# Optimization experiments

Hardware: AMD Instinct MI355X
Metric: run time of the kernel (lower is better)

Reference implementation:

```python
import jax, jax.numpy as jnp
import numpy as np

N = 50000
E = 400000
H1, H2, D = 4, 2, 64
NEG_SLOPE = 0.2
EPS = 1e-5


def _segment_softmax(alpha, dst, num_nodes):
    # alpha: [E, H], softmax over edges sharing the same dst node
    m = jax.ops.segment_max(alpha, dst, num_segments=num_nodes)  # [N, H]
    ex = jnp.exp(alpha - m[dst])
    den = jax.ops.segment_sum(ex, dst, num_segments=num_nodes)   # [N, H]
    return ex / den[dst]


def _gat_conv(x, src, dst, eattr, W, We, a_src, a_dst, a_edge, b, heads, num_nodes):
    # x: [N, Fin] -> h: [N, H, D]; eattr: [E, Fe] -> e: [E, H, D]
    h = (x @ W).reshape(num_nodes, heads, D)
    e = (eattr @ We).reshape(-1, heads, D)
    al_src = jnp.einsum('nhd,hd->nh', h, a_src)   # [N, H]
    al_dst = jnp.einsum('nhd,hd->nh', h, a_dst)   # [N, H]
    al_e = jnp.einsum('ehd,hd->eh', e, a_edge)    # [E, H]
    alpha = al_src[src] + al_dst[dst] + al_e
    alpha = jax.nn.leaky_relu(alpha, NEG_SLOPE)
    alpha = _segment_softmax(alpha, dst, num_nodes)
    msg = h[src] * alpha[:, :, None]              # [E, H, D]
    out = jax.ops.segment_sum(msg, dst, num_segments=num_nodes)
    return out.reshape(num_nodes, heads * D) + b


def _graph_norm(x, w, b, mean_scale):
    # PyG GraphNorm over the whole (single) graph
    mean = jnp.mean(x, axis=0, keepdims=True)
    out = x - mean * mean_scale
    var = jnp.mean(out * out, axis=0, keepdims=True)
    return w * out / jnp.sqrt(var + EPS) + b


def _forward(x, edge_index, edge_attr,
             W1, We1, as1, ad1, ae1, b1, gn1_w, gn1_b, gn1_ms,
             W2, We2, as2, ad2, ae2, b2, gn2_w, gn2_b, gn2_ms,
             Wc, bc):
    # add self loops (PyG default), self-loop edge_attr = mean of edge_attr
    loops = jnp.arange(N)
    src = jnp.concatenate([edge_index[0], loops])
    dst = jnp.concatenate([edge_index[1], loops])
    ea_mean = jnp.mean(edge_attr, axis=0, keepdims=True)
    eattr = jnp.concatenate([edge_attr, jnp.broadcast_to(ea_mean, (N, edge_attr.shape[1]))])

    h = _gat_conv(x, src, dst, eattr, W1, We1, as1, ad1, ae1, b1, H1, N)
    h = jax.nn.elu(_graph_norm(h, gn1_w, gn1_b, gn1_ms))
    h = _gat_conv(h, src, dst, eattr, W2, We2, as2, ad2, ae2, b2, H2, N)
    h = jax.nn.elu(_graph_norm(h, gn2_w, gn2_b, gn2_ms))
    return h @ Wc + bc


def setup_inputs() -> dict:
    key = jax.random.key(0)
    ks = jax.random.split(key, 20)
    g = lambda k, shape, fan: jax.random.normal(k, shape, jnp.float32) * (1.0 / np.sqrt(fan))
    inp = {
        'x': jax.random.normal(ks[0], (N, 3), jnp.float32),
        'edge_index': jax.random.randint(ks[1], (2, E), 0, N),
        'edge_attr': jax.random.uniform(ks[2], (E, 2), jnp.float32),
        'W1': g(ks[3], (3, H1 * D), 3),
        'We1': g(ks[4], (2, H1 * D), 2),
        'as1': g(ks[5], (H1, D), D),
        'ad1': g(ks[6], (H1, D), D),
        'ae1': g(ks[7], (H1, D), D),
        'b1': jnp.zeros((H1 * D,), jnp.float32),
        'gn1_w': jnp.ones((H1 * D,), jnp.float32),
        'gn1_b': jnp.zeros((H1 * D,), jnp.float32),
        'gn1_ms': jnp.ones((H1 * D,), jnp.float32),
        'W2': g(ks[8], (H1 * D, H2 * D), H1 * D),
        'We2': g(ks[9], (2, H2 * D), 2),
        'as2': g(ks[10], (H2, D), D),
        'ad2': g(ks[11], (H2, D), D),
        'ae2': g(ks[12], (H2, D), D),
        'b2': jnp.zeros((H2 * D,), jnp.float32),
        'gn2_w': jnp.ones((H2 * D,), jnp.float32),
        'gn2_b': jnp.zeros((H2 * D,), jnp.float32),
        'gn2_ms': jnp.ones((H2 * D,), jnp.float32),
        # classifier 128 -> 13
        'Wc': g(ks[13], (H2 * D, 13), H2 * D),
        'bc': jnp.zeros((13,), jnp.float32),
    }
    return inp


def reference(x, edge_index, edge_attr,
              W1, We1, as1, ad1, ae1, b1, gn1_w, gn1_b, gn1_ms,
              W2, We2, as2, ad2, ae2, b2, gn2_w, gn2_b, gn2_ms,
              Wc, bc):
    return _forward(x, edge_index, edge_attr,
                    W1, We1, as1, ad1, ae1, b1, gn1_w, gn1_b, gn1_ms,
                    W2, We2, as2, ad2, ae2, b2, gn2_w, gn2_b, gn2_ms,
                    Wc, bc)
```

## Files before the change

kernel.cpp:

```cpp
#include <hip/hip_runtime.h>
#include <math.h>

#define NEG_SLOPE 0.2f
#define GEPS 1e-5f

typedef __attribute__((ext_vector_type(8))) short short8;
typedef __attribute__((ext_vector_type(4))) float floatx4;

__device__ __forceinline__ float wave_reduce_sum(float v) {
#pragma unroll
    for (int o = 32; o > 0; o >>= 1) v += __shfl_down(v, o);
    return v;
}

__device__ __forceinline__ ushort f2bf(float f) {
    union { float f; unsigned int i; } c;
    c.f = f;
    unsigned int b = c.i;
    b += 0x7fffu + ((b >> 16) & 1u);
    return (ushort)(b >> 16);
}

__device__ __forceinline__ float bf2f(ushort u) {
    union { unsigned int i; float f; } c;
    c.i = (unsigned int)u << 16;
    return c.f;
}

__device__ __forceinline__ float2 unpack_bf2(unsigned int u) {
    union { unsigned int i; float f; } a, b;
    a.i = u << 16;
    b.i = u & 0xffff0000u;
    return make_float2(a.f, b.f);
}

__device__ __forceinline__ unsigned int pack_bf2(float lo, float hi) {
    return (unsigned int)f2bf(lo) | ((unsigned int)f2bf(hi) << 16);
}

__device__ __forceinline__ float lrelu(float v) {
    return (v > 0.f) ? v : v * NEG_SLOPE;
}

__device__ __forceinline__ float elu_fast(float v) {
    return (v > 0.f) ? v : (__expf(v) - 1.f);
}

__global__ __launch_bounds__(256) void k_pre(
    const float* __restrict__ W1, const float* __restrict__ as1, const float* __restrict__ ad1,
    const float* __restrict__ ea, const int* __restrict__ dst,
    const float* __restrict__ W2, const float* __restrict__ We1,
    const float* __restrict__ ae1, const float* __restrict__ We2,
    const float* __restrict__ ae2,
    float* __restrict__ ea_sum, int* __restrict__ deg, uint4* __restrict__ Bfrag,
    float* __restrict__ C1, float* __restrict__ C2, float* __restrict__ Ps,
    float* __restrict__ Pd, int E) {
    int b = blockIdx.x;
    if (b < 16) {
        int t = b * 256 + threadIdx.x;
        int c = t >> 9, kk = (t >> 6) & 7, L = t & 63;
        int q = L >> 4, n = c * 16 + (L & 15);
        int k0 = kk * 32 + q * 8;
        unsigned int u0 = pack_bf2(W2[(k0 + 0) * 128 + n], W2[(k0 + 1) * 128 + n]);
        unsigned int u1 = pack_bf2(W2[(k0 + 2) * 128 + n], W2[(k0 + 3) * 128 + n]);
        unsigned int u2 = pack_bf2(W2[(k0 + 4) * 128 + n], W2[(k0 + 5) * 128 + n]);
        unsigned int u3 = pack_bf2(W2[(k0 + 6) * 128 + n], W2[(k0 + 7) * 128 + n]);
        Bfrag[t] = make_uint4(u0, u1, u2, u3);
        return;
    }
    if (b == 16) {
        int t = threadIdx.x, h = t >> 6, lane = t & 63;
        float p0 = We1[t] * ae1[t];
        float p1 = We1[256 + t] * ae1[t];
        p0 = wave_reduce_sum(p0);
        p1 = wave_reduce_sum(p1);
        if (lane == 0) { C1[h] = p0; C1[4 + h] = p1; }
        float av = as1[t], dv = ad1[t];
#pragma unroll
        for (int k = 0; k < 3; ++k) {
            float wv = W1[k * 256 + t];
            float ps = wave_reduce_sum(wv * av);
            float pd = wave_reduce_sum(wv * dv);
            if (lane == 0) { Ps[h * 3 + k] = ps; Pd[h * 3 + k] = pd; }
        }
        if (t < 128) {
            float q0 = We2[t] * ae2[t];
            float q1 = We2[128 + t] * ae2[t];
            q0 = wave_reduce_sum(q0);
            q1 = wave_reduce_sum(q1);
            if (lane == 0) { C2[h] = q0; C2[2 + h] = q1; }
        }
        return;
    }
    b -= 17;
    const float2* ea2 = (const float2*)ea;
    float s0 = 0.f, s1 = 0.f;
    for (int e = b * 256 + threadIdx.x; e < E; e += 256 * 256) {
        float2 v = ea2[e];
        s0 += v.x; s1 += v.y;
        atomicAdd(&deg[dst[e]], 1);
    }
    s0 = wave_reduce_sum(s0);
    s1 = wave_reduce_sum(s1);
    if ((threadIdx.x & 63) == 0) {
        atomicAdd(&ea_sum[0], s0);
        atomicAdd(&ea_sum[1], s1);
    }
}

__global__ void k_scan1(const int* __restrict__ deg, int* __restrict__ row_ptr,
                        int* __restrict__ bsum, int N) {
    __shared__ int tmp[1024];
    int tid = threadIdx.x;
    int i = blockIdx.x * 1024 + tid;
    int v = (i < N) ? deg[i] : 0;
    tmp[tid] = v;
    __syncthreads();
#pragma unroll
    for (int off = 1; off < 1024; off <<= 1) {
        int t = (tid >= off) ? tmp[tid - off] : 0;
        __syncthreads();
        tmp[tid] += t;
        __syncthreads();
    }
    if (i < N) row_ptr[i + 1] = tmp[tid];
    if (tid == 1023) bsum[blockIdx.x] = tmp[1023];
}

__global__ void k_scan23(int* __restrict__ row_ptr, const int* __restrict__ bsum,
                         const float* __restrict__ ea_sum, const float* __restrict__ C1,
                         const float* __restrict__ C2, const float* __restrict__ Ps,
                         const float* __restrict__ Pd, const float* __restrict__ x,
                         float* __restrict__ al_s1, float* __restrict__ al_d1,
                         float* __restrict__ lE1, float* __restrict__ lE2, int N, int E) {
    __shared__ int off_s;
    int t = threadIdx.x;
    if (blockIdx.x == 0 && t >= 64 && t < 68) {
        int k = t - 64;
        float m0 = ea_sum[0] / (float)E, m1 = ea_sum[1] / (float)E;
        lE1[k] = m0 * C1[k] + m1 * C1[4 + k];
        if (k < 2) lE2[k] = m0 * C2[k] + m1 * C2[2 + k];
    }
    if (t < 64) {
        int v = (t < blockIdx.x) ? bsum[t] : 0;
#pragma unroll
        for (int o = 32; o > 0; o >>= 1) v += __shfl_xor(v, o);
        if (t == 0) off_s = v;
    }
    __syncthreads();
    int off = off_s;
    int i = blockIdx.x * 1024 + t;
    if (i == 0) row_ptr[0] = 0;
    if (i < N) {
        row_ptr[i + 1] += off;
        float x0 = x[3 * i], x1 = x[3 * i + 1], x2 = x[3 * i + 2];
        float4 sv, dv;
        sv.x = fmaf(x0, Ps[0], fmaf(x1, Ps[1], x2 * Ps[2]));
        sv.y = fmaf(x0, Ps[3], fmaf(x1, Ps[4], x2 * Ps[5]));
        sv.z = fmaf(x0, Ps[6], fmaf(x1, Ps[7], x2 * Ps[8]));
        sv.w = fmaf(x0, Ps[9], fmaf(x1, Ps[10], x2 * Ps[11]));
        dv.x = fmaf(x0, Pd[0], fmaf(x1, Pd[1], x2 * Pd[2]));
        dv.y = fmaf(x0, Pd[3], fmaf(x1, Pd[4], x2 * Pd[5]));
        dv.z = fmaf(x0, Pd[6], fmaf(x1, Pd[7], x2 * Pd[8]));
        dv.w = fmaf(x0, Pd[9], fmaf(x1, Pd[10], x2 * Pd[11]));
        *(float4*)(al_s1 + 4 * (size_t)i) = sv;
        *(float4*)(al_d1 + 4 * (size_t)i) = dv;
    }
}

__global__ void k_scatfill(const int* __restrict__ dst, const int* __restrict__ src,
                           const float* __restrict__ ea, const int* __restrict__ row_ptr,
                           int* __restrict__ deg, const float* __restrict__ al_s1,
                           const float* __restrict__ al_d1, const float* __restrict__ C1,
                           float2* __restrict__ ea2, uint4* __restrict__ wmp, int E) {
    int e = blockIdx.x * 256 + threadIdx.x;
    if (e >= E) return;
    int d = dst[e];
    int r = atomicSub(&deg[d], 1);
    int slot = row_ptr[d] + r - 1;
    int s = src[e];
    float2 v = ((const float2*)ea)[e];
    float4 as = *(const float4*)(al_s1 + 4 * (size_t)s);
    float4 ad = *(const float4*)(al_d1 + 4 * (size_t)d);
    float w0 = __expf(lrelu(as.x + ad.x + v.x * C1[0] + v.y * C1[4]));
    float w1 = __expf(lrelu(as.y + ad.y + v.x * C1[1] + v.y * C1[5]));
    float w2 = __expf(lrelu(as.z + ad.z + v.x * C1[2] + v.y * C1[6]));
    float w3 = __expf(lrelu(as.w + ad.w + v.x * C1[3] + v.y * C1[7]));
    ea2[slot] = v;
    wmp[slot] = make_uint4((unsigned int)s, pack_bf2(w0, w1), pack_bf2(w2, w3), 0u);
}

__global__ __launch_bounds__(256) void k_agg1(const float* __restrict__ x,
                                              const int* __restrict__ row_ptr,
                                              const uint4* __restrict__ wmp,
                                              const float* __restrict__ al_s,
                                              const float* __restrict__ al_d,
                                              const float* __restrict__ lE,
                                              const float* __restrict__ W1,
                                              const float* __restrict__ bias,
                                              ushort* __restrict__ out, int N) {
    int l = threadIdx.x & 31;
    int grp = threadIdx.x >> 5;
    int n = blockIdx.x * 8 + grp;
    if (n >= N) return;
    int c0 = l * 8;
    int hh = l >> 3;
    float4 wa0 = *(const float4*)(W1 + c0);
    float4 wa1 = *(const float4*)(W1 + c0 + 4);
    float4 wb0 = *(const float4*)(W1 + 256 + c0);
    float4 wb1 = *(const float4*)(W1 + 256 + c0 + 4);
    float4 wc0 = *(const float4*)(W1 + 512 + c0);
    float4 wc1 = *(const float4*)(W1 + 512 + c0 + 4);
    float4 bv0 = *(const float4*)(bias + c0);
    float4 bv1 = *(const float4*)(bias + c0 + 4);
    float4 asn = *(const float4*)(al_s + 4 * (size_t)n);
    float4 adn = *(const float4*)(al_d + 4 * (size_t)n);
    float ws0 = __expf(lrelu(asn.x + adn.x + lE[0]));
    float ws1 = __expf(lrelu(asn.y + adn.y + lE[1]));
    float ws2 = __expf(lrelu(asn.z + adn.z + lE[2]));
    float ws3 = __expf(lrelu(asn.w + adn.w + lE[3]));
    float z[12];
    float ds[4];
#pragma unroll
    for (int k = 0; k < 12; ++k) z[k] = 0.f;
#pragma unroll
    for (int k = 0; k < 4; ++k) ds[k] = 0.f;
    int i0 = row_ptr[n];
    int cnt = row_ptr[n + 1] - i0;
    for (int j = l; j < cnt; j += 32) {
        uint4 me = wmp[i0 + j];
        int s = (int)me.x;
        float xs0 = x[3 * s], xs1 = x[3 * s + 1], xs2 = x[3 * s + 2];
        float2 w01 = unpack_bf2(me.y);
        float2 w23 = unpack_bf2(me.z);
        z[0] = fmaf(w01.x, xs0, z[0]); z[1] = fmaf(w01.x, xs1, z[1]); z[2] = fmaf(w01.x, xs2, z[2]);
        z[3] = fmaf(w01.y, xs0, z[3]); z[4] = fmaf(w01.y, xs1, z[4]); z[5] = fmaf(w01.y, xs2, z[5]);
        z[6] = fmaf(w23.x, xs0, z[6]); z[7] = fmaf(w23.x, xs1, z[7]); z[8] = fmaf(w23.x, xs2, z[8]);
        z[9] = fmaf(w23.y, xs0, z[9]); z[10] = fmaf(w23.y, xs1, z[10]); z[11] = fmaf(w23.y, xs2, z[11]);
        ds[0] += w01.x; ds[1] += w01.y; ds[2] += w23.x; ds[3] += w23.y;
    }
    bool hi16 = (l & 16) != 0;
    float a0, a1, a2, a3, a4, a5, a6, a7, gv, rv;
    gv = hi16 ? z[0] : z[6];  rv = __shfl_xor(gv, 16); a0 = (hi16 ? z[6] : z[0]) + rv;
    gv = hi16 ? z[1] : z[7];  rv = __shfl_xor(gv, 16); a1 = (hi16 ? z[7] : z[1]) + rv;
    gv = hi16 ? z[2] : z[8];  rv = __shfl_xor(gv, 16); a2 = (hi16 ? z[8] : z[2]) + rv;
    gv = hi16 ? z[3] : z[9];  rv = __shfl_xor(gv, 16); a3 = (hi16 ? z[9] : z[3]) + rv;
    gv = hi16 ? z[4] : z[10]; rv = __shfl_xor(gv, 16); a4 = (hi16 ? z[10] : z[4]) + rv;
    gv = hi16 ? z[5] : z[11]; rv = __shfl_xor(gv, 16); a5 = (hi16 ? z[11] : z[5]) + rv;
    gv = hi16 ? ds[0] : ds[2]; rv = __shfl_xor(gv, 16); a6 = (hi16 ? ds[2] : ds[0]) + rv;
    gv = hi16 ? ds[1] : ds[3]; rv = __shfl_xor(gv, 16); a7 = (hi16 ? ds[3] : ds[1]) + rv;
    bool hi8 = (l & 8) != 0;
    float c0v, c1v, c2v, c3v;
    gv = hi8 ? a0 : a3; rv = __shfl_xor(gv, 8); c0v = (hi8 ? a3 : a0) + rv;
    gv = hi8 ? a1 : a4; rv = __shfl_xor(gv, 8); c1v = (hi8 ? a4 : a1) + rv;
    gv = hi8 ? a2 : a5; rv = __shfl_xor(gv, 8); c2v = (hi8 ? a5 : a2) + rv;
    gv = hi8 ? a6 : a7; rv = __shfl_xor(gv, 8); c3v = (hi8 ? a7 : a6) + rv;
#pragma unroll
    for (int o = 4; o > 0; o >>= 1) {
        c0v += __shfl_xor(c0v, o);
        c1v += __shfl_xor(c1v, o);
        c2v += __shfl_xor(c2v, o);
        c3v += __shfl_xor(c3v, o);
    }
    float wsh = (hh == 0) ? ws0 : (hh == 1) ? ws1 : (hh == 2) ? ws2 : ws3;
    float xn0 = x[3 * n], xn1 = x[3 * n + 1], xn2 = x[3 * n + 2];
    c0v = fmaf(wsh, xn0, c0v);
    c1v = fmaf(wsh, xn1, c1v);
    c2v = fmaf(wsh, xn2, c2v);
    c3v += wsh;
    float inv = 1.f / c3v;
    float v0 = fmaf(fmaf(c0v, wa0.x, fmaf(c1v, wb0.x, c2v * wc0.x)), inv, bv0.x);
    float v1 = fmaf(fmaf(c0v, wa0.y, fmaf(c1v, wb0.y, c2v * wc0.y)), inv, bv0.y);
    float v2 = fmaf(fmaf(c0v, wa0.z, fmaf(c1v, wb0.z, c2v * wc0.z)), inv, bv0.z);
    float v3 = fmaf(fmaf(c0v, wa0.w, fmaf(c1v, wb0.w, c2v * wc0.w)), inv, bv0.w);
    float v4 = fmaf(fmaf(c0v, wa1.x, fmaf(c1v, wb1.x, c2v * wc1.x)), inv, bv1.x);
    float v5 = fmaf(fmaf(c0v, wa1.y, fmaf(c1v, wb1.y, c2v * wc1.y)), inv, bv1.y);
    float v6 = fmaf(fmaf(c0v, wa1.z, fmaf(c1v, wb1.z, c2v * wc1.z)), inv, bv1.z);
    float v7 = fmaf(fmaf(c0v, wa1.w, fmaf(c1v, wb1.w, c2v * wc1.w)), inv, bv1.w);
    uint4 o;
    o.x = pack_bf2(v0, v1);
    o.y = pack_bf2(v2, v3);
    o.z = pack_bf2(v4, v5);
    o.w = pack_bf2(v6, v7);
    ((uint4*)out)[(size_t)n * 32 + l] = o;
}

__global__ __launch_bounds__(256) void k_agg2(const ushort* __restrict__ h2,
                                              const int* __restrict__ row_ptr,
                                              const uint4* __restrict__ wmp,
                                              const float2* __restrict__ ea2,
                                              const float* __restrict__ al_s,
                                              const float* __restrict__ al_d,
                                              const float* __restrict__ C2,
                                              const float* __restrict__ lE,
                                              const float* __restrict__ bias,
                                              ushort* __restrict__ out, int N) {
    int n = blockIdx.x * 4 + (threadIdx.x >> 6);
    if (n >= N) return;
    int lane = threadIdx.x & 63;
    int g = lane >> 4, c16 = lane & 15;
    bool hi = c16 >= 8;
    const uint4* h2u4 = (const uint4*)h2;
    float2 ad = *(const float2*)(al_d + 2 * (size_t)n);
    float2 as = *(const float2*)(al_s + 2 * (size_t)n);
    float wsA = __expf(lrelu(as.x + ad.x + lE[0]));
    float wsB = __expf(lrelu(as.y + ad.y + lE[1]));
    float c2x = hi ? C2[1] : C2[0];
    float c2y = hi ? C2[3] : C2[2];
    float adh = hi ? ad.y : ad.x;
    uint4 hs = h2u4[(size_t)n * 16 + c16];
    float wself = (g == 0) ? (hi ? wsB : wsA) : 0.f;
    float dsum = wself;
    float acc[8];
    {
        float2 t0 = unpack_bf2(hs.x), t1 = unpack_bf2(hs.y);
        float2 t2 = unpack_bf2(hs.z), t3 = unpack_bf2(hs.w);
        acc[0] = wself * t0.x; acc[1] = wself * t0.y;
        acc[2] = wself * t1.x; acc[3] = wself * t1.y;
        acc[4] = wself * t2.x; acc[5] = wself * t2.y;
        acc[6] = wself * t3.x; acc[7] = wself * t3.y;
    }
    int i0 = row_ptr[n];
    int cnt = row_ptr[n + 1] - i0;
    if (cnt > 0) {
        int last = cnt - 1;
        int nit = (cnt + 3) >> 2;
        int j0 = g;      float mkA = 1.f; if (j0 > last) { j0 = last; mkA = 0.f; }
        int j1 = 4 + g;  float mkB = 1.f; if (j1 > last) { j1 = last; mkB = 0.f; }
        int j2 = 8 + g;  float mkC = 1.f; if (j2 > last) { j2 = last; mkC = 0.f; }
        int j3 = 12 + g; float mkD = 1.f; if (j3 > last) { j3 = last; mkD = 0.f; }
        uint4 meA = wmp[i0 + j0]; float2 eaA = ea2[i0 + j0];
        uint4 meB = wmp[i0 + j1]; float2 eaB = ea2[i0 + j1];
        uint4 meC = wmp[i0 + j2]; float2 eaC = ea2[i0 + j2];
        uint4 meD = wmp[i0 + j3]; float2 eaD = ea2[i0 + j3];
        float2 alA = *(const float2*)(al_s + 2 * (size_t)meA.x);
        uint4 gvA = h2u4[(size_t)meA.x * 16 + c16];
        float2 alB = *(const float2*)(al_s + 2 * (size_t)meB.x);
        uint4 gvB = h2u4[(size_t)meB.x * 16 + c16];
        float2 alC = *(const float2*)(al_s + 2 * (size_t)meC.x);
        uint4 gvC = h2u4[(size_t)meC.x * 16 + c16];
        for (int it = 0; it < nit - 1; ++it) {
            float2 alD = *(const float2*)(al_s + 2 * (size_t)meD.x);
            uint4 gvD = h2u4[(size_t)meD.x * 16 + c16];
            int jn = 4 * (it + 4) + g;
            float mn = 1.f;
            if (jn > last) { jn = last; mn = 0.f; }
            uint4 meE = wmp[i0 + jn]; float2 eaE = ea2[i0 + jn];
            float lg = (hi ? alA.y : alA.x) + adh + eaA.x * c2x + eaA.y * c2y;
            float wg = __expf(lrelu(lg)) * mkA;
            dsum += wg;
            float2 u;
            u = unpack_bf2(gvA.x); acc[0] = fmaf(wg, u.x, acc[0]); acc[1] = fmaf(wg, u.y, acc[1]);
            u = unpack_bf2(gvA.y); acc[2] = fmaf(wg, u.x, acc[2]); acc[3] = fmaf(wg, u.y, acc[3]);
            u = unpack_bf2(gvA.z); acc[4] = fmaf(wg, u.x, acc[4]); acc[5] = fmaf(wg, u.y, acc[5]);
            u = unpack_bf2(gvA.w); acc[6] = fmaf(wg, u.x, acc[6]); acc[7] = fmaf(wg, u.y, acc[7]);
            meA = meB; meB = meC; meC = meD; meD = meE;
            eaA = eaB; eaB = eaC; eaC = eaD; eaD = eaE;
            alA = alB; alB = alC; alC = alD;
            gvA = gvB; gvB = gvC; gvC = gvD;
            mkA = mkB; mkB = mkC; mkC = mkD; mkD = mn;
        }
        float lg = (hi ? alA.y : alA.x) + adh + eaA.x * c2x + eaA.y * c2y;
        float wg = __expf(lrelu(lg)) * mkA;
        dsum += wg;
        float2 u;
        u = unpack_bf2(gvA.x); acc[0] = fmaf(wg, u.x, acc[0]); acc[1] = fmaf(wg, u.y, acc[1]);
        u = unpack_bf2(gvA.y); acc[2] = fmaf(wg, u.x, acc[2]); acc[3] = fmaf(wg, u.y, acc[3]);
        u = unpack_bf2(gvA.z); acc[4] = fmaf(wg, u.x, acc[4]); acc[5] = fmaf(wg, u.y, acc[5]);
        u = unpack_bf2(gvA.w); acc[6] = fmaf(wg, u.x, acc[6]); acc[7] = fmaf(wg, u.y, acc[7]);
    }
#pragma unroll
    for (int k = 0; k < 8; ++k) {
        acc[k] += __shfl_xor(acc[k], 16);
        acc[k] += __shfl_xor(acc[k], 32);
    }
    dsum += __shfl_xor(dsum, 16);
    dsum += __shfl_xor(dsum, 32);
    if (g == 0) {
        float inv = 1.f / dsum;
        const float* bp = bias + c16 * 8;
        float4 b0 = *(const float4*)bp;
        float4 b1 = *(const float4*)(bp + 4);
        uint4 o;
        o.x = pack_bf2(fmaf(acc[0], inv, b0.x), fmaf(acc[1], inv, b0.y));
        o.y = pack_bf2(fmaf(acc[2], inv, b0.z), fmaf(acc[3], inv, b0.w));
        o.z = pack_bf2(fmaf(acc[4], inv, b1.x), fmaf(acc[5], inv, b1.y));
        o.w = pack_bf2(fmaf(acc[6], inv, b1.z), fmaf(acc[7], inv, b1.w));
        ((uint4*)out)[(size_t)n * 16 + c16] = o;
    }
}

template <int C4>
__global__ __launch_bounds__(256) void k_stats_bf(const ushort* __restrict__ x,
                                                  float* __restrict__ stats, int rows) {
    const int C = C4 * 8;
    const int RG = 256 / C4;
    int t = threadIdx.x;
    int c = t & (C4 - 1);
    int rg = t / C4;
    int rpb = (rows + gridDim.x - 1) / gridDim.x;
    int r0 = blockIdx.x * rpb;
    int r1 = r0 + rpb;
    if (r1 > rows) r1 = rows;
    const uint4* xu = (const uint4*)x;
    float s[8] = {0.f, 0.f, 0.f, 0.f, 0.f, 0.f, 0.f, 0.f};
    float q[8] = {0.f, 0.f, 0.f, 0.f, 0.f, 0.f, 0.f, 0.f};
    for (int r = r0 + rg; r < r1; r += RG) {
        uint4 v = xu[(size_t)r * C4 + c];
        float2 a0 = unpack_bf2(v.x), a1 = unpack_bf2(v.y);
        float2 a2 = unpack_bf2(v.z), a3 = unpack_bf2(v.w);
        s[0] += a0.x; q[0] = fmaf(a0.x, a0.x, q[0]);
        s[1] += a0.y; q[1] = fmaf(a0.y, a0.y, q[1]);
        s[2] += a1.x; q[2] = fmaf(a1.x, a1.x, q[2]);
        s[3] += a1.y; q[3] = fmaf(a1.y, a1.y, q[3]);
        s[4] += a2.x; q[4] = fmaf(a2.x, a2.x, q[4]);
        s[5] += a2.y; q[5] = fmaf(a2.y, a2.y, q[5]);
        s[6] += a3.x; q[6] = fmaf(a3.x, a3.x, q[6]);
        s[7] += a3.y; q[7] = fmaf(a3.y, a3.y, q[7]);
    }
    __shared__ float ls[256 * 16];
#pragma unroll
    for (int k = 0; k < 8; ++k) {
        ls[t * 16 + k] = s[k];
        ls[t * 16 + 8 + k] = q[k];
    }
    __syncthreads();
    if (t < C) {
        int cc = t >> 3, k = t & 7;
        float ssum = 0.f, qsum = 0.f;
#pragma unroll
        for (int g = 0; g < RG; ++g) {
            ssum += ls[(g * C4 + cc) * 16 + k];
            qsum += ls[(g * C4 + cc) * 16 + 8 + k];
        }
        atomicAdd(&stats[t], ssum);
        atomicAdd(&stats[C + t], qsum);
    }
}

__global__ __launch_bounds__(256) void k_gemm2_mfma(const ushort* __restrict__ X,
                                                    const float* __restrict__ stats,
                                                    const float* __restrict__ gw,
                                                    const float* __restrict__ gb,
                                                    const float* __restrict__ gms,
                                                    const uint4* __restrict__ Bfrag,
                                                    const float* __restrict__ as2,
                                                    const float* __restrict__ ad2,
                                                    ushort* __restrict__ H2,
                                                    float* __restrict__ al_s,
                                                    float* __restrict__ al_d, int Nn) {
    __shared__ __align__(16) float ABs[512];
    {
        int t = threadIdx.x;
        float inv = 1.f / (float)Nn;
        float mean = stats[t] * inv;
        float cm = mean * gms[t];
        float var = stats[256 + t] * inv - 2.f * cm * mean + cm * cm;
        float A = gw[t] * rsqrtf(var + GEPS);
        ABs[t] = A;
        ABs[256 + t] = gb[t] - A * cm;
    }
    __syncthreads();
    int wave = threadIdx.x >> 6, lane = threadIdx.x & 63;
    int q = lane >> 4, m = lane & 15;
    int rowbase = blockIdx.x * 64 + wave * 16;
    int row = rowbase + m;
    bool valid = row < Nn;
    const uint4* xr4 = (const uint4*)((const unsigned int*)X + (size_t)row * 128);
    uint4 xa[8];
#pragma unroll
    for (int kk = 0; kk < 8; ++kk) {
        int k0 = kk * 32 + q * 8;
        xa[kk] = valid ? xr4[k0 >> 3] : make_uint4(0, 0, 0, 0);
    }
    union { short8 s; unsigned int u[4]; } af[8];
#pragma unroll
    for (int kk = 0; kk < 8; ++kk) {
        int k0 = kk * 32 + q * 8;
        float2 x01 = unpack_bf2(xa[kk].x);
        float2 x23 = unpack_bf2(xa[kk].y);
        float2 x45 = unpack_bf2(xa[kk].z);
        float2 x67 = unpack_bf2(xa[kk].w);
        float4 a0 = *(const float4*)(ABs + k0);
        float4 a1 = *(const float4*)(ABs + k0 + 4);
        float4 b0 = *(const float4*)(ABs + 256 + k0);
        float4 b1 = *(const float4*)(ABs + 256 + k0 + 4);
        float v0 = elu_fast(fmaf(a0.x, x01.x, b0.x));
        float v1 = elu_fast(fmaf(a0.y, x01.y, b0.y));
        float v2 = elu_fast(fmaf(a0.z, x23.x, b0.z));
        float v3 = elu_fast(fmaf(a0.w, x23.y, b0.w));
        float v4 = elu_fast(fmaf(a1.x, x45.x, b1.x));
        float v5 = elu_fast(fmaf(a1.y, x45.y, b1.y));
        float v6 = elu_fast(fmaf(a1.z, x67.x, b1.z));
        float v7 = elu_fast(fmaf(a1.w, x67.y, b1.w));
        af[kk].u[0] = pack_bf2(v0, v1);
        af[kk].u[1] = pack_bf2(v2, v3);
        af[kk].u[2] = pack_bf2(v4, v5);
        af[kk].u[3] = pack_bf2(v6, v7);
    }
    floatx4 acc[8];
#pragma unroll
    for (int c = 0; c < 8; ++c) acc[c] = (floatx4){0.f, 0.f, 0.f, 0.f};
#pragma unroll
    for (int kk = 0; kk < 8; ++kk) {
        const uint4* bpf = Bfrag + kk * 64 + lane;
#pragma unroll
        for (int c = 0; c < 8; ++c) {
            union { short8 s; uint4 u; } bf;
            bf.u = bpf[c * 8 * 64];
            acc[c] = __builtin_amdgcn_mfma_f32_16x16x32_bf16(af[kk].s, bf.s, acc[c], 0, 0, 0);
        }
    }
    float a_s[8], a_d[8];
#pragma unroll
    for (int c = 0; c < 8; ++c) {
        a_s[c] = as2[c * 16 + m];
        a_d[c] = ad2[c * 16 + m];
    }
#pragma unroll
    for (int r = 0; r < 4; ++r) {
        int orow = rowbase + q * 4 + r;
        bool vr = orow < Nn;
        ushort us[8];
        float s0 = 0.f, s1 = 0.f, d0 = 0.f, d1 = 0.f;
#pragma unroll
        for (int c = 0; c < 8; ++c) {
            us[c] = f2bf(acc[c][r]);
            float v = bf2f(us[c]);
            if (c < 4) {
                s0 = fmaf(v, a_s[c], s0);
                d0 = fmaf(v, a_d[c], d0);
            } else {
                s1 = fmaf(v, a_s[c], s1);
                d1 = fmaf(v, a_d[c], d1);
            }
        }
#pragma unroll
        for (int o = 1; o < 16; o <<= 1) {
            s0 += __shfl_xor(s0, o);
            s1 += __shfl_xor(s1, o);
            d0 += __shfl_xor(d0, o);
            d1 += __shfl_xor(d1, o);
        }
        if (vr) {
            ushort* op = H2 + (size_t)orow * 128 + m;
#pragma unroll
            for (int c = 0; c < 8; ++c) op[c * 16] = us[c];
            if (m == 0) {
                *(float2*)(al_s + 2 * (size_t)orow) = make_float2(s0, s1);
                *(float2*)(al_d + 2 * (size_t)orow) = make_float2(d0, d1);
            }
        }
    }
}

__global__ __launch_bounds__(256) void k_cls(const ushort* __restrict__ X,
                                             const float* __restrict__ stats,
                                             const float* __restrict__ gw,
                                             const float* __restrict__ gb,
                                             const float* __restrict__ gms,
                                             const float* __restrict__ Wc,
                                             const float* __restrict__ bc,
                                             float* __restrict__ out, int Nn) {
    __shared__ __align__(16) float ls[16 * 132];
    __shared__ __align__(16) float wT[13 * 132];
    __shared__ __align__(16) float ABs[256];
    __shared__ float bS[13];
    int t = threadIdx.x;
    int n0 = blockIdx.x * 16;
    if (t < 128) {
        float inv = 1.f / (float)Nn;
        float mean = stats[t] * inv;
        float cm = mean * gms[t];
        float var = stats[128 + t] * inv - 2.f * cm * mean + cm * cm;
        float A = gw[t] * rsqrtf(var + GEPS);
        ABs[t] = A;
        ABs[128 + t] = gb[t] - A * cm;
    }
    for (int i = t; i < 128 * 13; i += 256) {
        int k = i / 13, j = i - k * 13;
        wT[j * 132 + k] = Wc[i];
    }
    if (t < 13) bS[t] = bc[t];
    __syncthreads();
    const unsigned int* xu = (const unsigned int*)X;
    for (int idx = t; idx < 16 * 64; idx += 256) {
        int r = idx >> 6, ku = idx & 63;
        int row = n0 + r;
        float vx = 0.f, vy = 0.f;
        if (row < Nn) {
            float2 v = unpack_bf2(xu[(size_t)row * 64 + ku]);
            int k = 2 * ku;
            vx = elu_fast(fmaf(ABs[k], v.x, ABs[128 + k]));
            vy = elu_fast(fmaf(ABs[k + 1], v.y, ABs[128 + k + 1]));
        }
        ls[r * 132 + 2 * ku] = vx;
        ls[r * 132 + 2 * ku + 1] = vy;
    }
    __syncthreads();
    if (t < 208) {
        int r = t / 13, j = t - r * 13;
        int row = n0 + r;
        if (row < Nn) {
            float acc = bS[j];
            const float* lr = &ls[r * 132];
            const float* wr = &wT[j * 132];
#pragma unroll 8
            for (int k = 0; k < 128; k += 4) {
                float4 a = *(const float4*)&lr[k];
                float4 b = *(const float4*)&wr[k];
                acc = fmaf(a.x, b.x, fmaf(a.y, b.y, fmaf(a.z, b.z, fmaf(a.w, b.w, acc))));
            }
            out[(size_t)row * 13 + j] = acc;
        }
    }
}

extern "C" void kernel_launch(void* const* d_in, const int* in_sizes, int n_in, void* d_out,
                              int out_size, void* d_ws, size_t ws_size, hipStream_t stream) {
    const float* x = (const float*)d_in[0];
    const int* edge_index = (const int*)d_in[1];
    const float* edge_attr = (const float*)d_in[2];
    const float* W1 = (const float*)d_in[3];
    const float* We1 = (const float*)d_in[4];
    const float* as1 = (const float*)d_in[5];
    const float* ad1 = (const float*)d_in[6];
    const float* ae1 = (const float*)d_in[7];
    const float* b1 = (const float*)d_in[8];
    const float* gn1_w = (const float*)d_in[9];
    const float* gn1_b = (const float*)d_in[10];
    const float* gn1_ms = (const float*)d_in[11];
    const float* W2 = (const float*)d_in[12];
    const float* We2 = (const float*)d_in[13];
    const float* as2 = (const float*)d_in[14];
    const float* ad2 = (const float*)d_in[15];
    const float* ae2 = (const float*)d_in[16];
    const float* b2 = (const float*)d_in[17];
    const float* gn2_w = (const float*)d_in[18];
    const float* gn2_b = (const float*)d_in[19];
    const float* gn2_ms = (const float*)d_in[20];
    const float* Wc = (const float*)d_in[21];
    const float* bc = (const float*)d_in[22];

    const int N = in_sizes[0] / 3;
    const int E = in_sizes[1] / 2;
    const int* srcv = edge_index;
    const int* dstv = edge_index + E;

    char* w = (char*)d_ws;
    auto carveB = [&](size_t bytes) -> void* {
        void* p = (void*)w;
        w += ((bytes + 255) / 256) * 256;
        return p;
    };
    int* deg = (int*)carveB((size_t)N * 4);
    float* ea_sum = (float*)carveB(8);
    float* statsA = (float*)carveB(512 * 4);
    float* statsB = (float*)carveB(256 * 4);
    char* zero_end = w;
    int* row_ptr = (int*)carveB((size_t)(N + 1) * 4);
    int* bsum = (int*)carveB(1024 * 4);
    float2* ea2 = (float2*)carveB((size_t)E * 8);
    uint4* wmp = (uint4*)carveB((size_t)E * 16);
    float* C1 = (float*)carveB(8 * 4);
    float* C2 = (float*)carveB(4 * 4);
    float* Ps = (float*)carveB(12 * 4);
    float* Pd = (float*)carveB(12 * 4);
    float* lE1 = (float*)carveB(4 * 4);
    float* lE2 = (float*)carveB(2 * 4);
    uint4* Bfrag = (uint4*)carveB(4096 * 16);
    float* al_s1 = (float*)carveB((size_t)N * 4 * 4);
    float* al_d1 = (float*)carveB((size_t)N * 4 * 4);
    float* al_s2 = (float*)carveB((size_t)N * 2 * 4);
    float* al_d2 = (float*)carveB((size_t)N * 2 * 4);
    ushort* h2b = (ushort*)carveB((size_t)N * 128 * 2);
    ushort* out1b = (ushort*)carveB((size_t)N * 256 * 2);
    ushort* out2b = (ushort*)carveB((size_t)N * 128 * 2);

    hipMemsetAsync(deg, 0, (size_t)(zero_end - (char*)deg), stream);

    const int nb1 = (N + 1023) / 1024;
    const int ebl = (E + 255) / 256;

    k_pre<<<17 + 256, 256, 0, stream>>>(W1, as1, ad1, edge_attr, dstv, W2, We1, ae1, We2, ae2,
                                        ea_sum, deg, Bfrag, C1, C2, Ps, Pd, E);
    k_scan1<<<nb1, 1024, 0, stream>>>(deg, row_ptr, bsum, N);
    k_scan23<<<nb1, 1024, 0, stream>>>(row_ptr, bsum, ea_sum, C1, C2, Ps, Pd, x, al_s1, al_d1,
                                       lE1, lE2, N, E);
    k_scatfill<<<ebl, 256, 0, stream>>>(dstv, srcv, edge_attr, row_ptr, deg, al_s1, al_d1, C1,
                                        ea2, wmp, E);
    k_agg1<<<(N + 7) / 8, 256, 0, stream>>>(x, row_ptr, wmp, al_s1, al_d1, lE1, W1, b1, out1b,
                                            N);
    k_stats_bf<32><<<256, 256, 0, stream>>>(out1b, statsA, N);
    k_gemm2_mfma<<<(N + 63) / 64, 256, 0, stream>>>(out1b, statsA, gn1_w, gn1_b, gn1_ms, Bfrag,
                                                    as2, ad2, h2b, al_s2, al_d2, N);
    k_agg2<<<(N + 3) / 4, 256, 0, stream>>>(h2b, row_ptr, wmp, ea2, al_s2, al_d2, C2, lE2, b2,
                                            out2b, N);
    k_stats_bf<16><<<256, 256, 0, stream>>>(out2b, statsB, N);
    k_cls<<<(N + 15) / 16, 256, 0, stream>>>(out2b, statsB, gn2_w, gn2_b, gn2_ms, Wc, bc,
                                             (float*)d_out, N);
}
```

Baseline: 277.0 us.

## Keep layer-1 output as 3-dim per-head aggregate and derive GraphNorm stats from moments

```diff
diff --git a/kernel.cpp b/kernel.cpp
--- a/kernel.cpp
+++ b/kernel.cpp
@@ -196,23 +196,12 @@
                                               const float* __restrict__ al_s,
                                               const float* __restrict__ al_d,
                                               const float* __restrict__ lE,
-                                              const float* __restrict__ W1,
-                                              const float* __restrict__ bias,
-                                              ushort* __restrict__ out, int N) {
+                                              float4* __restrict__ uarr, int N) {
     int l = threadIdx.x & 31;
     int grp = threadIdx.x >> 5;
     int n = blockIdx.x * 8 + grp;
     if (n >= N) return;
-    int c0 = l * 8;
     int hh = l >> 3;
-    float4 wa0 = *(const float4*)(W1 + c0);
-    float4 wa1 = *(const float4*)(W1 + c0 + 4);
-    float4 wb0 = *(const float4*)(W1 + 256 + c0);
-    float4 wb1 = *(const float4*)(W1 + 256 + c0 + 4);
-    float4 wc0 = *(const float4*)(W1 + 512 + c0);
-    float4 wc1 = *(const float4*)(W1 + 512 + c0 + 4);
-    float4 bv0 = *(const float4*)(bias + c0);
-    float4 bv1 = *(const float4*)(bias + c0 + 4);
     float4 asn = *(const float4*)(al_s + 4 * (size_t)n);
     float4 adn = *(const float4*)(al_d + 4 * (size_t)n);
     float ws0 = __expf(lrelu(asn.x + adn.x + lE[0]));
@@ -268,21 +257,148 @@
     c1v = fmaf(wsh, xn1, c1v);
     c2v = fmaf(wsh, xn2, c2v);
     c3v += wsh;
-    float inv = 1.f / c3v;
-    float v0 = fmaf(fmaf(c0v, wa0.x, fmaf(c1v, wb0.x, c2v * wc0.x)), inv, bv0.x);
-    float v1 = fmaf(fmaf(c0v, wa0.y, fmaf(c1v, wb0.y, c2v * wc0.y)), inv, bv0.y);
-    float v2 = fmaf(fmaf(c0v, wa0.z, fmaf(c1v, wb0.z, c2v * wc0.z)), inv, bv0.z);
-    float v3 = fmaf(fmaf(c0v, wa0.w, fmaf(c1v, wb0.w, c2v * wc0.w)), inv, bv0.w);
-    float v4 = fmaf(fmaf(c0v, wa1.x, fmaf(c1v, wb1.x, c2v * wc1.x)), inv, bv1.x);
-    float v5 = fmaf(fmaf(c0v, wa1.y, fmaf(c1v, wb1.y, c2v * wc1.y)), inv, bv1.y);
-    float v6 = fmaf(fmaf(c0v, wa1.z, fmaf(c1v, wb1.z, c2v * wc1.z)), inv, bv1.z);
-    float v7 = fmaf(fmaf(c0v, wa1.w, fmaf(c1v, wb1.w, c2v * wc1.w)), inv, bv1.w);
-    uint4 o;
-    o.x = pack_bf2(v0, v1);
-    o.y = pack_bf2(v2, v3);
-    o.z = pack_bf2(v4, v5);
-    o.w = pack_bf2(v6, v7);
-    ((uint4*)out)[(size_t)n * 32 + l] = o;
+    if ((l & 7) == 0) {
+        float inv = 1.f / c3v;
+        uarr[(size_t)n * 4 + hh] = make_float4(c0v * inv, c1v * inv, c2v * inv, 0.f);
+    }
+}
+
+__global__ __launch_bounds__(256) void k_mom(const float4* __restrict__ uarr,
+                                             float* __restrict__ mom, int N4) {
+    int t = threadIdx.x;
+    float m[9] = {0.f, 0.f, 0.f, 0.f, 0.f, 0.f, 0.f, 0.f, 0.f};
+    for (int i = blockIdx.x * 256 + t; i < N4; i += gridDim.x * 256) {
+        float4 u = uarr[i];
+        m[0] += u.x; m[1] += u.y; m[2] += u.z;
+        m[3] = fmaf(u.x, u.x, m[3]);
+        m[4] = fmaf(u.y, u.y, m[4]);
+        m[5] = fmaf(u.z, u.z, m[5]);
+        m[6] = fmaf(u.x, u.y, m[6]);
+        m[7] = fmaf(u.x, u.z, m[7]);
+        m[8] = fmaf(u.y, u.z, m[8]);
+    }
+    __shared__ float ls[256 * 9];
+#pragma unroll
+    for (int k = 0; k < 9; ++k) ls[t * 9 + k] = m[k];
+    __syncthreads();
+    if (t < 36) {
+        int h = t / 9, k = t - h * 9;
+        float s = 0.f;
+        for (int tt = h; tt < 256; tt += 4) s += ls[tt * 9 + k];
+        atomicAdd(&mom[t], s);
+    }
+}
+
+__global__ __launch_bounds__(256) void k_gemm2_mfma(const float4* __restrict__ uarr,
+                                                    const float* __restrict__ mom,
+                                                    const float* __restrict__ W1,
+                                                    const float* __restrict__ b1,
+                                                    const float* __restrict__ gw,
+                                                    const float* __restrict__ gb,
+                                                    const float* __restrict__ gms,
+                                                    const uint4* __restrict__ Bfrag,
+                                                    const float* __restrict__ as2,
+                                                    const float* __restrict__ ad2,
+                                                    ushort* __restrict__ H2,
+                                                    float* __restrict__ al_s,
+                                                    float* __restrict__ al_d, int Nn) {
+    __shared__ __align__(16) float4 Wc4[256];
+    __shared__ __align__(16) float2 ABs2[256];
+    __shared__ __align__(16) float4 Uld[256];
+    {
+        int t = threadIdx.x;
+        float w0 = W1[t], w1 = W1[256 + t], w2 = W1[512 + t], bb = b1[t];
+        Wc4[t] = make_float4(w0, w1, w2, bb);
+        const float* mh = mom + (t >> 6) * 9;
+        float invN = 1.f / (float)Nn;
+        float sw = w0 * mh[0] + w1 * mh[1] + w2 * mh[2];
+        float mean = fmaf(sw, invN, bb);
+        float quad = w0 * w0 * mh[3] + w1 * w1 * mh[4] + w2 * w2 * mh[5] +
+                     2.f * (w0 * w1 * mh[6] + w0 * w2 * mh[7] + w1 * w2 * mh[8]);
+        float E2 = fmaf(fmaf(2.f * bb, sw, quad), invN, bb * bb);
+        float cm = mean * gms[t];
+        float var = E2 - 2.f * cm * mean + cm * cm;
+        float A = gw[t] * rsqrtf(var + GEPS);
+        ABs2[t] = make_float2(A, gb[t] - A * cm);
+        int row = blockIdx.x * 64 + (t >> 2);
+        Uld[t] = (row < Nn) ? uarr[(size_t)row * 4 + (t & 3)] : make_float4(0.f, 0.f, 0.f, 0.f);
+    }
+    __syncthreads();
+    int wave = threadIdx.x >> 6, lane = threadIdx.x & 63;
+    int q = lane >> 4, m = lane & 15;
+    int rowbase = blockIdx.x * 64 + wave * 16;
+    union { short8 s; unsigned int u[4]; } af[8];
+#pragma unroll
+    for (int kk = 0; kk < 8; ++kk) {
+        float4 u = Uld[(wave * 16 + m) * 4 + (kk >> 1)];
+        int c0 = kk * 32 + q * 8;
+        float vv[8];
+#pragma unroll
+        for (int j = 0; j < 8; ++j) {
+            float4 wv = Wc4[c0 + j];
+            float2 ab = ABs2[c0 + j];
+            float X = fmaf(u.x, wv.x, fmaf(u.y, wv.y, fmaf(u.z, wv.z, wv.w)));
+            vv[j] = elu_fast(fmaf(ab.x, X, ab.y));
+        }
+        af[kk].u[0] = pack_bf2(vv[0], vv[1]);
+        af[kk].u[1] = pack_bf2(vv[2], vv[3]);
+        af[kk].u[2] = pack_bf2(vv[4], vv[5]);
+        af[kk].u[3] = pack_bf2(vv[6], vv[7]);
+    }
+    floatx4 acc[8];
+#pragma unroll
+    for (int c = 0; c < 8; ++c) acc[c] = (floatx4){0.f, 0.f, 0.f, 0.f};
+#pragma unroll
+    for (int kk = 0; kk < 8; ++kk) {
+        const uint4* bpf = Bfrag + kk * 64 + lane;
+#pragma unroll
+        for (int c = 0; c < 8; ++c) {
+            union { short8 s; uint4 u; } bf;
+            bf.u = bpf[c * 8 * 64];
+            acc[c] = __builtin_amdgcn_mfma_f32_16x16x32_bf16(af[kk].s, bf.s, acc[c], 0, 0, 0);
+        }
+    }
+    float a_s[8], a_d[8];
+#pragma unroll
+    for (int c = 0; c < 8; ++c) {
+        a_s[c] = as2[c * 16 + m];
+        a_d[c] = ad2[c * 16 + m];
+    }
+#pragma unroll
+    for (int r = 0; r < 4; ++r) {
+        int orow = rowbase + q * 4 + r;
+        bool vr = orow < Nn;
+        ushort us[8];
+        float s0 = 0.f, s1 = 0.f, d0 = 0.f, d1 = 0.f;
+#pragma unroll
+        for (int c = 0; c < 8; ++c) {
+            us[c] = f2bf(acc[c][r]);
+            float v = bf2f(us[c]);
+            if (c < 4) {
+                s0 = fmaf(v, a_s[c], s0);
+                d0 = fmaf(v, a_d[c], d0);
+            } else {
+                s1 = fmaf(v, a_s[c], s1);
+                d1 = fmaf(v, a_d[c], d1);
+            }
+        }
+#pragma unroll
+        for (int o = 1; o < 16; o <<= 1) {
+            s0 += __shfl_xor(s0, o);
+            s1 += __shfl_xor(s1, o);
+            d0 += __shfl_xor(d0, o);
+            d1 += __shfl_xor(d1, o);
+        }
+        if (vr) {
+            ushort* op = H2 + (size_t)orow * 128 + m;
+#pragma unroll
+            for (int c = 0; c < 8; ++c) op[c * 16] = us[c];
+            if (m == 0) {
+                *(float2*)(al_s + 2 * (size_t)orow) = make_float2(s0, s1);
+                *(float2*)(al_d + 2 * (size_t)orow) = make_float2(d0, d1);
+            }
+        }
+    }
 }
 
 __global__ __launch_bounds__(256) void k_agg2(const ushort* __restrict__ h2,
@@ -438,122 +554,6 @@
     }
 }
 
-__global__ __launch_bounds__(256) void k_gemm2_mfma(const ushort* __restrict__ X,
-                                                    const float* __restrict__ stats,
-                                                    const float* __restrict__ gw,
-                                                    const float* __restrict__ gb,
-                                                    const float* __restrict__ gms,
-                                                    const uint4* __restrict__ Bfrag,
-                                                    const float* __restrict__ as2,
-                                                    const float* __restrict__ ad2,
-                                                    ushort* __restrict__ H2,
-                                                    float* __restrict__ al_s,
-                                                    float* __restrict__ al_d, int Nn) {
-    __shared__ __align__(16) float ABs[512];
-    {
-        int t = threadIdx.x;
-        float inv = 1.f / (float)Nn;
-        float mean = stats[t] * inv;
-        float cm = mean * gms[t];
-        float var = stats[256 + t] * inv - 2.f * cm * mean + cm * cm;
-        float A = gw[t] * rsqrtf(var + GEPS);
-        ABs[t] = A;
-        ABs[256 + t] = gb[t] - A * cm;
-    }
-    __syncthreads();
-    int wave = threadIdx.x >> 6, lane = threadIdx.x & 63;
-    int q = lane >> 4, m = lane & 15;
-    int rowbase = blockIdx.x * 64 + wave * 16;
-    int row = rowbase + m;
-    bool valid = row < Nn;
-    const uint4* xr4 = (const uint4*)((const unsigned int*)X + (size_t)row * 128);
-    uint4 xa[8];
-#pragma unroll
-    for (int kk = 0; kk < 8; ++kk) {
-        int k0 = kk * 32 + q * 8;
-        xa[kk] = valid ? xr4[k0 >> 3] : make_uint4(0, 0, 0, 0);
-    }
-    union { short8 s; unsigned int u[4]; } af[8];
-#pragma unroll
-    for (int kk = 0; kk < 8; ++kk) {
-        int k0 = kk * 32 + q * 8;
-        float2 x01 = unpack_bf2(xa[kk].x);
-        float2 x23 = unpack_bf2(xa[kk].y);
-        float2 x45 = unpack_bf2(xa[kk].z);
-        float2 x67 = unpack_bf2(xa[kk].w);
-        float4 a0 = *(const float4*)(ABs + k0);
-        float4 a1 = *(const float4*)(ABs + k0 + 4);
-        float4 b0 = *(const float4*)(ABs + 256 + k0);
-        float4 b1 = *(const float4*)(ABs + 256 + k0 + 4);
-        float v0 = elu_fast(fmaf(a0.x, x01.x, b0.x));
-        float v1 = elu_fast(fmaf(a0.y, x01.y, b0.y));
-        float v2 = elu_fast(fmaf(a0.z, x23.x, b0.z));
-        float v3 = elu_fast(fmaf(a0.w, x23.y, b0.w));
-        float v4 = elu_fast(fmaf(a1.x, x45.x, b1.x));
-        float v5 = elu_fast(fmaf(a1.y, x45.y, b1.y));
-        float v6 = elu_fast(fmaf(a1.z, x67.x, b1.z));
-        float v7 = elu_fast(fmaf(a1.w, x67.y, b1.w));
-        af[kk].u[0] = pack_bf2(v0, v1);
-        af[kk].u[1] = pack_bf2(v2, v3);
-        af[kk].u[2] = pack_bf2(v4, v5);
-        af[kk].u[3] = pack_bf2(v6, v7);
-    }
-    floatx4 acc[8];
-#pragma unroll
-    for (int c = 0; c < 8; ++c) acc[c] = (floatx4){0.f, 0.f, 0.f, 0.f};
-#pragma unroll
-    for (int kk = 0; kk < 8; ++kk) {
-        const uint4* bpf = Bfrag + kk * 64 + lane;
-#pragma unroll
-        for (int c = 0; c < 8; ++c) {
-            union { short8 s; uint4 u; } bf;
-            bf.u = bpf[c * 8 * 64];
-            acc[c] = __builtin_amdgcn_mfma_f32_16x16x32_bf16(af[kk].s, bf.s, acc[c], 0, 0, 0);
-        }
-    }
-    float a_s[8], a_d[8];
-#pragma unroll
-    for (int c = 0; c < 8; ++c) {
-        a_s[c] = as2[c * 16 + m];
-        a_d[c] = ad2[c * 16 + m];
-    }
-#pragma unroll
-    for (int r = 0; r < 4; ++r) {
-        int orow = rowbase + q * 4 + r;
-        bool vr = orow < Nn;
-        ushort us[8];
-        float s0 = 0.f, s1 = 0.f, d0 = 0.f, d1 = 0.f;
-#pragma unroll
-        for (int c = 0; c < 8; ++c) {
-            us[c] = f2bf(acc[c][r]);
-            float v = bf2f(us[c]);
-            if (c < 4) {
-                s0 = fmaf(v, a_s[c], s0);
-                d0 = fmaf(v, a_d[c], d0);
-            } else {
-                s1 = fmaf(v, a_s[c], s1);
-                d1 = fmaf(v, a_d[c], d1);
-            }
-        }
-#pragma unroll
-        for (int o = 1; o < 16; o <<= 1) {
-            s0 += __shfl_xor(s0, o);
-            s1 += __shfl_xor(s1, o);
-            d0 += __shfl_xor(d0, o);
-            d1 += __shfl_xor(d1, o);
-        }
-        if (vr) {
-            ushort* op = H2 + (size_t)orow * 128 + m;
-#pragma unroll
-            for (int c = 0; c < 8; ++c) op[c * 16] = us[c];
-            if (m == 0) {
-                *(float2*)(al_s + 2 * (size_t)orow) = make_float2(s0, s1);
-                *(float2*)(al_d + 2 * (size_t)orow) = make_float2(d0, d1);
-            }
-        }
-    }
-}
-
 __global__ __launch_bounds__(256) void k_cls(const ushort* __restrict__ X,
                                              const float* __restrict__ stats,
                                              const float* __restrict__ gw,
@@ -655,7 +655,7 @@
     };
     int* deg = (int*)carveB((size_t)N * 4);
     float* ea_sum = (float*)carveB(8);
-    float* statsA = (float*)carveB(512 * 4);
+    float* mom = (float*)carveB(36 * 4);
     float* statsB = (float*)carveB(256 * 4);
     char* zero_end = w;
     int* row_ptr = (int*)carveB((size_t)(N + 1) * 4);
@@ -673,8 +673,8 @@
     float* al_d1 = (float*)carveB((size_t)N * 4 * 4);
     float* al_s2 = (float*)carveB((size_t)N * 2 * 4);
     float* al_d2 = (float*)carveB((size_t)N * 2 * 4);
+    float4* uarr = (float4*)carveB((size_t)N * 4 * 16);
     ushort* h2b = (ushort*)carveB((size_t)N * 128 * 2);
-    ushort* out1b = (ushort*)carveB((size_t)N * 256 * 2);
     ushort* out2b = (ushort*)carveB((size_t)N * 128 * 2);
 
     hipMemsetAsync(deg, 0, (size_t)(zero_end - (char*)deg), stream);
@@ -689,11 +689,10 @@
                                        lE1, lE2, N, E);
     k_scatfill<<<ebl, 256, 0, stream>>>(dstv, srcv, edge_attr, row_ptr, deg, al_s1, al_d1, C1,
                                         ea2, wmp, E);
-    k_agg1<<<(N + 7) / 8, 256, 0, stream>>>(x, row_ptr, wmp, al_s1, al_d1, lE1, W1, b1, out1b,
-                                            N);
-    k_stats_bf<32><<<256, 256, 0, stream>>>(out1b, statsA, N);
-    k_gemm2_mfma<<<(N + 63) / 64, 256, 0, stream>>>(out1b, statsA, gn1_w, gn1_b, gn1_ms, Bfrag,
-                                                    as2, ad2, h2b, al_s2, al_d2, N);
+    k_agg1<<<(N + 7) / 8, 256, 0, stream>>>(x, row_ptr, wmp, al_s1, al_d1, lE1, uarr, N);
+    k_mom<<<128, 256, 0, stream>>>(uarr, mom, N * 4);
+    k_gemm2_mfma<<<(N + 63) / 64, 256, 0, stream>>>(uarr, mom, W1, b1, gn1_w, gn1_b, gn1_ms,
+                                                    Bfrag, as2, ad2, h2b, al_s2, al_d2, N);
     k_agg2<<<(N + 3) / 4, 256, 0, stream>>>(h2b, row_ptr, wmp, ea2, al_s2, al_d2, C2, lE2, b2,
                                             out2b, N);
     k_stats_bf<16><<<256, 256, 0, stream>>>(out2b, statsB, N);
```

Measured after the change: 265.8 us. -4.1%, faster.
